# Optimization experiments

Hardware: AMD Instinct MI355X
Metric: run time of the kernel (lower is better)

Reference implementation:

```python
import jax, jax.numpy as jnp
import numpy as np
from jax import lax

B, C, D, H, W = 2, 256, 32, 64, 192
TRAIN_W = 640
DISPS = np.arange(D, dtype=np.float32) * 0.01  # norm_disp_range


def conv1x1(x, w, b):
    # x [B,Cin,H,W], w [Cout,Cin]
    return jnp.einsum('bchw,oc->bohw', x, w) + b[None, :, None, None]


def conv3x3(x, w, b):
    y = lax.conv_general_dilated(x, w, (1, 1), 'SAME',
                                 dimension_numbers=('NCHW', 'OIHW', 'NCHW'))
    return y + b[None, :, None, None]


def warp_volume(x, shift_px):
    """Horizontal bilinear warp with border clamp for each disparity.
    x [B,Cc,H,W], shift_px [B,D] (pixel shift) -> [B,Cc,D,H,W]."""
    Wd = x.shape[3]
    j = jnp.arange(Wd, dtype=x.dtype)
    src = jnp.clip(j[None, None, :] + shift_px[:, :, None], 0.0, Wd - 1.0)  # [B,D,W]
    x0 = jnp.floor(src).astype(jnp.int32)
    x1 = jnp.minimum(x0 + 1, Wd - 1)
    frac = src - x0.astype(src.dtype)  # [B,D,W]

    def one(xb, i0, i1, fb):
        g0 = xb[:, :, i0]  # [Cc,H,D,W]
        g1 = xb[:, :, i1]
        out = g0 * (1.0 - fb) + g1 * fb
        return out.transpose(0, 2, 1, 3)  # [Cc,D,H,W]

    return jax.vmap(one)(x, x0, x1, frac)


def setup_inputs() -> dict:
    key = jax.random.key(0)
    ks = jax.random.split(key, 16)
    f32 = jnp.float32
    inp = {
        't_feat': jax.random.normal(ks[0], (B, C, H, W), f32),
        's_feat': jax.random.normal(ks[1], (B, C, H, W), f32),
        'directs': jnp.ones((B, 1, 1, 1), f32),
        'qw': jax.random.normal(ks[2], (C // 4, C), f32) * 0.05,
        'qb': jax.random.normal(ks[3], (C // 4,), f32) * 0.05,
        'kw': jax.random.normal(ks[4], (C // 4, C), f32) * 0.05,
        'kb': jax.random.normal(ks[5], (C // 4,), f32) * 0.05,
        'vw': jax.random.normal(ks[6], (C // 4, C), f32) * 0.05,
        'vb': jax.random.normal(ks[7], (C // 4,), f32) * 0.05,
        'p1w': jax.random.normal(ks[8], (C // 4, C // 2, 3, 3), f32) * 0.05,
        'p1b': jax.random.normal(ks[9], (C // 4,), f32) * 0.05,
        'p2w': jax.random.normal(ks[10], (D, C // 4, 3, 3), f32) * 0.05,
        'p2b': jax.random.normal(ks[11], (D,), f32) * 0.05,
        'rw': jax.random.normal(ks[12], (C, C + D), f32) * 0.05,
        'rb': jax.random.normal(ks[13], (C,), f32) * 0.05,
        'img_w': TRAIN_W,
    }
    return inp


def reference(t_feat, s_feat, directs, qw, qb, kw, kb, vw, vb,
              p1w, p1b, p2w, p2b, rw, rb, img_w):
    rel_scale = (TRAIN_W / img_w) if img_w != TRAIN_W else 1.0
    q = conv1x1(t_feat, qw, qb)  # [B,C/4,H,W]
    k = conv1x1(s_feat, kw, kb)
    v = conv1x1(s_feat, vw, vb)

    Wd = t_feat.shape[3]
    disps = jnp.asarray(DISPS, t_feat.dtype)
    # normalized shift d*2*rel_scale*directs -> pixels: * (W-1)/2
    shift = disps[None, :] * rel_scale * directs.reshape(-1, 1) * (Wd - 1)  # [B,D]

    wk = warp_volume(k, shift)  # [B,C/4,D,H,W]
    wv = warp_volume(v, shift)

    cq = q.shape[1]
    cost = jnp.einsum('bchw,bcdhw->bdhw', q, wk) / (cq ** 0.5)  # [B,D,H,W]
    norm_cost = jax.nn.softmax(cost, axis=1)
    agg_v = jnp.einsum('bdhw,bcdhw->bchw', norm_cost, wv)  # [B,C/4,H,W]

    h1 = jax.nn.elu(conv3x3(jnp.concatenate([q, agg_v], axis=1), p1w, p1b))
    res_cost = conv3x3(h1, p2w, p2b)  # [B,D,H,W]
    cost = (cost + res_cost) * 0.5
    norm_cost = jax.nn.softmax(cost, axis=1)
    x = jax.nn.elu(conv1x1(jnp.concatenate([t_feat, norm_cost], axis=1), rw, rb))
    return x, cost
```

## Files before the change

### kernel.cpp

```cpp
#include <hip/hip_runtime.h>

#define BB 2
#define CC 256
#define CQ 64
#define DD 32
#define HH 64
#define WW 192
#define HW (HH*WW)
#define NPIX (BB*HW)

typedef __attribute__((ext_vector_type(8))) short bf16x8;
typedef __attribute__((ext_vector_type(4))) float f32x4;

__device__ __forceinline__ float b2f(ushort s){ return __uint_as_float(((uint)s)<<16); }
__device__ __forceinline__ ushort f2b(float f){
    uint u = __float_as_uint(f);
    return (ushort)((u + 0x7fffu + ((u>>16)&1u)) >> 16);
}
__device__ __forceinline__ float eluf(float v){ return v > 0.f ? v : (__expf(v)-1.f); }

__global__ __launch_bounds__(256) void k_prep_feat(
    const float* __restrict__ t_feat, const float* __restrict__ s_feat,
    ushort* __restrict__ Tt, ushort* __restrict__ Ts)
{
    __shared__ ushort sT[64*264];
    int blk = blockIdx.x;
    int which = blk / 384;
    int rem   = blk % 384;
    int b     = rem / 192;
    int tile  = rem % 192;
    int p0    = tile*64;
    const float* src = which ? s_feat : t_feat;
    ushort* dst      = which ? Ts : Tt;
    int tid = threadIdx.x;

    for (int i = tid; i < 2048; i += 256){
        int px  = i & 63;
        int c16 = i >> 6;
        const float* p = src + ((size_t)(b*CC + c16*8))*HW + p0 + px;
        uint u[4];
        #pragma unroll
        for (int j2=0;j2<4;++j2)
            u[j2] = (uint)f2b(p[(size_t)(2*j2)*HW]) | ((uint)f2b(p[(size_t)(2*j2+1)*HW])<<16);
        uint4 q4; q4.x=u[0]; q4.y=u[1]; q4.z=u[2]; q4.w=u[3];
        *(uint4*)&sT[(px*33 + c16)*8] = q4;
    }
    __syncthreads();
    for (int i = tid; i < 2048; i += 256){
        int c16 = i & 31;
        int px  = i >> 5;
        uint4 v = *(const uint4*)&sT[(px*33 + c16)*8];
        *(uint4*)(dst + ((size_t)(b*HW + p0 + px))*CC + c16*8) = v;
    }
}

__global__ __launch_bounds__(256) void k_prep_w(
    const float* __restrict__ qw, const float* __restrict__ qb,
    const float* __restrict__ kw, const float* __restrict__ kb,
    const float* __restrict__ vw, const float* __restrict__ vb,
    const float* __restrict__ p1w, const float* __restrict__ p2w,
    const float* __restrict__ rw,
    ushort* __restrict__ Wqkv, float* __restrict__ bqkv,
    ushort* __restrict__ A1, ushort* __restrict__ A2, ushort* __restrict__ Ar)
{
    int id = blockIdx.x*256 + threadIdx.x;
    if (id < 49152) {
        int o = id / 256, c = id % 256;
        float v = (o<64)? qw[o*256+c] : (o<128)? kw[(o-64)*256+c] : vw[(o-128)*256+c];
        Wqkv[id] = f2b(v);
    } else if (id < 49344) {
        int o = id - 49152;
        bqkv[o] = (o<64)? qb[o] : (o<128)? kb[o-64] : vb[o-128];
    } else if (id < 49344+73728) {
        int i = id - 49344;
        int o = i/1152, r = i%1152, t = r/128, ci = r%128;
        A1[i] = f2b(p1w[(size_t)(o*128+ci)*9 + t]);
    } else if (id < 49344+73728+18432) {
        int i = id - (49344+73728);
        int o = i/576, r = i%576, t = r/64, ci = r%64;
        A2[i] = f2b(p2w[(size_t)(o*64+ci)*9 + t]);
    } else if (id < 49344+73728+18432+73728) {
        int i = id - (49344+73728+18432);
        Ar[i] = f2b(rw[i]);
    }
}

__global__ __launch_bounds__(256) void g_qkv(
    const ushort* __restrict__ Tt, const ushort* __restrict__ Ts,
    const ushort* __restrict__ Wqkv, const float* __restrict__ bqkv,
    ushort* __restrict__ X1, ushort* __restrict__ Vb)
{
    __shared__ ushort sT[32*264];
    __shared__ ushort sS[32*264];
    int tid = threadIdx.x;
    int bid = blockIdx.x;
    int tile = (bid & 7)*96 + (bid >> 3);
    int p0 = tile * 32;

    for (int i = tid; i < 1024; i += 256){
        int px = i >> 5, c16 = i & 31;
        size_t gsrc = ((size_t)(p0 + px))*CC + c16*8;
        *(uint4*)&sT[(px*33 + c16)*8] = *(const uint4*)(Tt + gsrc);
        *(uint4*)&sS[(px*33 + c16)*8] = *(const uint4*)(Ts + gsrc);
    }
    __syncthreads();

    int wv = tid >> 6, lane = tid & 63;
    int lm = lane & 15, lk = lane >> 4;
    f32x4 acc[3][2];
    #pragma unroll
    for (int g=0;g<3;++g){ acc[g][0]=(f32x4){0.f,0.f,0.f,0.f}; acc[g][1]=(f32x4){0.f,0.f,0.f,0.f}; }
    const ushort* Ap = Wqkv + (size_t)(wv*16 + lm)*CC + lk*8;

    #pragma unroll
    for (int k0=0; k0<CC; k0+=32){
        bf16x8 a0 = *(const bf16x8*)(Ap + k0);
        bf16x8 a1 = *(const bf16x8*)(Ap + 64*CC + k0);
        bf16x8 a2 = *(const bf16x8*)(Ap + 128*CC + k0);
        #pragma unroll
        for (int nt=0; nt<2; ++nt){
            int ch = (nt*16+lm)*33 + (k0>>3) + lk;
            bf16x8 bT = *(const bf16x8*)&sT[ch*8];
            bf16x8 bS = *(const bf16x8*)&sS[ch*8];
            acc[0][nt] = __builtin_amdgcn_mfma_f32_16x16x32_bf16(a0, bT, acc[0][nt], 0,0,0);
            acc[1][nt] = __builtin_amdgcn_mfma_f32_16x16x32_bf16(a1, bS, acc[1][nt], 0,0,0);
            acc[2][nt] = __builtin_amdgcn_mfma_f32_16x16x32_bf16(a2, bS, acc[2][nt], 0,0,0);
        }
    }
    int ol = wv*16 + lk*4;
    #pragma unroll
    for (int g=0;g<3;++g){
        int ob = g*64 + ol;
        #pragma unroll
        for (int nt=0; nt<2; ++nt){
            int p = p0 + nt*16 + lm;
            uint u0 = (uint)f2b(acc[g][nt][0]+bqkv[ob])   | ((uint)f2b(acc[g][nt][1]+bqkv[ob+1])<<16);
            uint u1 = (uint)f2b(acc[g][nt][2]+bqkv[ob+2]) | ((uint)f2b(acc[g][nt][3]+bqkv[ob+3])<<16);
            ushort* dst;
            if (g==0)      dst = X1 + (size_t)p*128 + ol;
            else if (g==1) dst = X1 + (size_t)p*128 + 64 + ol;
            else           dst = Vb + (size_t)p*64 + ol;
            *(uint2*)dst = make_uint2(u0, u1);
        }
    }
}

#define BAND 160
#define SROW 161
#define PROW 168
__global__ __launch_bounds__(512) void k_ca(
    const ushort* __restrict__ X1, const ushort* __restrict__ Vb,
    const float* __restrict__ directs, const int* __restrict__ img_w_p,
    float* __restrict__ C1, ushort* __restrict__ Agg)
{
    __shared__ ushort sQ[32*64];
    __shared__ ushort sK[BAND*64];
    __shared__ ushort sV[BAND*64];
    __shared__ float  sS[32*SROW];
    __shared__ ushort sPC[32*PROW];
    int tid = threadIdx.x;
    int j   = blockIdx.x;
    int r8  = j & 7;
    int kk  = j >> 3;
    int sub = kk % 6;
    int rhi = kk / 6;
    int row = rhi*8 + r8;
    int b   = row >> 6;
    int h   = row & 63;
    int w0  = sub * 32;
    size_t rowbase = (size_t)b*HW + (size_t)h*WW;

    for (int i = tid; i < BAND*8; i += 512){
        int x = i >> 3, c8 = i & 7;
        int gx = w0 - 64 + x;
        uint4 kv = make_uint4(0,0,0,0), vv = make_uint4(0,0,0,0);
        if (gx >= 0 && gx < WW){
            kv = *(const uint4*)(X1 + (rowbase+gx)*128 + 64 + c8*8);
            vv = *(const uint4*)(Vb + (rowbase+gx)*64 + c8*8);
        }
        int sw = (x*8 + (c8 ^ (x&7)))*8;
        *(uint4*)&sK[sw] = kv;
        *(uint4*)&sV[sw] = vv;
    }
    if (tid < 256){
        int px = tid >> 3, c8 = tid & 7;
        uint4 qv = *(const uint4*)(X1 + (rowbase + w0 + px)*128 + c8*8);
        *(uint4*)&sQ[(px*8 + (c8 ^ (px&7)))*8] = qv;
    }
    __syncthreads();

    int w8 = tid >> 6, lane = tid & 63;
    int lm = lane & 15, lk = lane >> 4;

    {
        int mt = w8 & 1;
        int qrow = mt*16 + lm;
        for (int nt = (w8 >> 1); nt < 10; nt += 4){
            int xrow = nt*16 + lm;
            f32x4 acc = {0.f,0.f,0.f,0.f};
            #pragma unroll
            for (int kt=0; kt<2; ++kt){
                bf16x8 a = *(const bf16x8*)&sQ[(qrow*8 + ((kt*4+lk) ^ (qrow&7)))*8];
                bf16x8 bbf = *(const bf16x8*)&sK[(xrow*8 + ((kt*4+lk) ^ (xrow&7)))*8];
                acc = __builtin_amdgcn_mfma_f32_16x16x32_bf16(a, bbf, acc, 0,0,0);
            }
            #pragma unroll
            for (int jj=0; jj<4; ++jj)
                sS[(mt*16 + lk*4 + jj)*SROW + xrow] = acc[jj];
        }
    }
    __syncthreads();

    int px  = tid >> 4;
    int l16 = tid & 15;
    int w   = w0 + px;
    size_t n = rowbase + w;
    int imw = img_w_p[0];
    float rel = (imw != 640) ? (640.0f/(float)imw) : 1.0f;
    float sf = 0.01f * rel * directs[b] * 191.0f;
    float wf = (float)w;

    float cost[2]; int xi0[2], xi1[2]; float frk[2];
    #pragma unroll
    for (int t=0; t<2; ++t){
        int d = l16*2 + t;
        float srcx = fminf(fmaxf(wf + (float)d*sf, 0.f), 191.0f);
        int x0 = (int)floorf(srcx);
        int x1 = min(x0+1, WW-1);
        float fr = srcx - (float)x0;
        int i0 = min(max(x0 - w0 + 64, 0), BAND-1);
        int i1 = min(max(x1 - w0 + 64, 0), BAND-1);
        xi0[t] = i0; xi1[t] = i1; frk[t] = fr;
        float s0 = sS[px*SROW + i0];
        float s1 = sS[px*SROW + i1];
        cost[t] = (s0 + fr*(s1-s0)) * 0.125f;
    }
    *(float2*)(C1 + n*DD + l16*2) = make_float2(cost[0], cost[1]);
    float mm = fmaxf(cost[0], cost[1]);
    mm = fmaxf(mm, __shfl_xor(mm, 1));
    mm = fmaxf(mm, __shfl_xor(mm, 2));
    mm = fmaxf(mm, __shfl_xor(mm, 4));
    mm = fmaxf(mm, __shfl_xor(mm, 8));
    float e0 = __expf(cost[0]-mm), e1 = __expf(cost[1]-mm);
    float ss = e0 + e1;
    ss += __shfl_xor(ss, 1);
    ss += __shfl_xor(ss, 2);
    ss += __shfl_xor(ss, 4);
    ss += __shfl_xor(ss, 8);
    float inv = 1.f/ss;
    float p0 = e0*inv, p1 = e1*inv;
    __syncthreads();

    for (int i = tid; i < 32*SROW; i += 512) sS[i] = 0.f;
    __syncthreads();

    {
        float w1a = p0*frk[0], w0a = p0 - w1a;
        float w1b = p1*frk[1], w0b = p1 - w1b;
        atomicAdd(&sS[px*SROW + xi0[0]], w0a);
        atomicAdd(&sS[px*SROW + xi1[0]], w1a);
        atomicAdd(&sS[px*SROW + xi0[1]], w0b);
        atomicAdd(&sS[px*SROW + xi1[1]], w1b);
    }
    __syncthreads();

    #pragma unroll
    for (int q=0; q<10; ++q){
        int xi = l16 + q*16;
        sPC[px*PROW + xi] = f2b(sS[px*SROW + xi]);
    }
    __syncthreads();

    {
        int mi = w8 & 3;
        int ni = w8 >> 2;
        int c  = mi*16 + lm;
        int wr = ni*16 + lm;
        f32x4 acc = {0.f,0.f,0.f,0.f};
        for (int kt=0; kt<5; ++kt){
            bf16x8 a;
            #pragma unroll
            for (int jj=0; jj<8; ++jj){
                int x = kt*32 + lk*8 + jj;
                a[jj] = (short)sV[(x*8 + ((c>>3) ^ (x&7)))*8 + (c&7)];
            }
            bf16x8 bbf = *(const bf16x8*)&sPC[wr*PROW + kt*32 + lk*8];
            acc = __builtin_amdgcn_mfma_f32_16x16x32_bf16(a, bbf, acc, 0,0,0);
        }
        uint u0 = (uint)f2b(acc[0]) | ((uint)f2b(acc[1])<<16);
        uint u1 = (uint)f2b(acc[2]) | ((uint)f2b(acc[3])<<16);
        *(uint2*)(Agg + (rowbase + w0 + wr)*64 + mi*16 + lk*4) = make_uint2(u0, u1);
    }
}

__global__ __launch_bounds__(256) void g_conv1(
    const ushort* __restrict__ X1, const ushort* __restrict__ Agg,
    const ushort* __restrict__ A1, const float* __restrict__ p1b,
    ushort* __restrict__ X2)
{
    __shared__ ushort sB[3*16*34*8];
    int tid = threadIdx.x;
    int wv = tid >> 6, lane = tid & 63;
    int lm = lane & 15, lk = lane >> 4;
    int bid = blockIdx.x;
    int tile = (bid & 7)*96 + (bid >> 3);
    int n0 = tile * 32;
    int b  = n0 / HW;
    int pl = n0 % HW;
    int h  = pl / WW, w0 = pl % WW;

    for (int i = tid; i < 1632; i += 256){
        int dh = i / 544, rem2 = i % 544;
        int c16 = rem2 / 34, x = rem2 % 34;
        int hh = h + dh - 1, wx = w0 + x - 1;
        uint4 val = make_uint4(0,0,0,0);
        if (hh >= 0 && hh < HH && wx >= 0 && wx < WW){
            size_t pix = (size_t)b*HW + (size_t)hh*WW + wx;
            val = (c16 < 8) ? *(const uint4*)(X1 + pix*128 + c16*8)
                            : *(const uint4*)(Agg + pix*64 + (c16-8)*8);
        }
        *(uint4*)&sB[((dh*16 + c16)*34 + x)*8] = val;
    }
    __syncthreads();

    int mw = wv & 1, nw = wv >> 1;
    const ushort* Ap = A1 + (size_t)(mw*32 + lm)*1152 + lk*8;
    f32x4 acc0 = {0.f,0.f,0.f,0.f}, acc1 = {0.f,0.f,0.f,0.f};
    int xb = nw*16 + lm;
    #pragma unroll
    for (int t=0; t<9; ++t){
        int dh = t/3, dw = t%3;
        #pragma unroll
        for (int c0=0; c0<128; c0+=32){
            bf16x8 bb = *(const bf16x8*)&sB[((dh*16 + (c0>>3)+lk)*34 + xb + dw)*8];
            bf16x8 a0 = *(const bf16x8*)(Ap + t*128 + c0);
            bf16x8 a1 = *(const bf16x8*)(Ap + (size_t)16*1152 + t*128 + c0);
            acc0 = __builtin_amdgcn_mfma_f32_16x16x32_bf16(a0, bb, acc0, 0,0,0);
            acc1 = __builtin_amdgcn_mfma_f32_16x16x32_bf16(a1, bb, acc1, 0,0,0);
        }
    }
    int pg = n0 + nw*16 + lm;
    int o0 = mw*32 + lk*4;
    {
        uint u0 = (uint)f2b(eluf(acc0[0]+p1b[o0]))   | ((uint)f2b(eluf(acc0[1]+p1b[o0+1]))<<16);
        uint u1 = (uint)f2b(eluf(acc0[2]+p1b[o0+2])) | ((uint)f2b(eluf(acc0[3]+p1b[o0+3]))<<16);
        *(uint2*)(X2 + (size_t)pg*64 + o0) = make_uint2(u0, u1);
        int o1 = o0 + 16;
        uint u2 = (uint)f2b(eluf(acc1[0]+p1b[o1]))   | ((uint)f2b(eluf(acc1[1]+p1b[o1+1]))<<16);
        uint u3 = (uint)f2b(eluf(acc1[2]+p1b[o1+2])) | ((uint)f2b(eluf(acc1[3]+p1b[o1+3]))<<16);
        *(uint2*)(X2 + (size_t)pg*64 + o1) = make_uint2(u2, u3);
    }
}

__global__ __launch_bounds__(256) void g_conv2(
    const ushort* __restrict__ X2, const ushort* __restrict__ A2,
    const float* __restrict__ p2b, const float* __restrict__ C1,
    float* __restrict__ cost_out)
{
    __shared__ ushort sB[3*8*34*8];
    int tid = threadIdx.x;
    int wv = tid >> 6, lane = tid & 63;
    int lm = lane & 15, lk = lane >> 4;
    int bid = blockIdx.x;
    int tile = (bid & 7)*96 + (bid >> 3);
    int n0 = tile * 32;
    int b  = n0 / HW;
    int pl = n0 % HW;
    int h  = pl / WW, w0 = pl % WW;

    for (int i = tid; i < 816; i += 256){
        int dh = i / 272, rem2 = i % 272;
        int c16 = rem2 / 34, x = rem2 % 34;
        int hh = h + dh - 1, wx = w0 + x - 1;
        uint4 val = make_uint4(0,0,0,0);
        if (hh >= 0 && hh < HH && wx >= 0 && wx < WW)
            val = *(const uint4*)(X2 + ((size_t)b*HW + (size_t)hh*WW + wx)*64 + c16*8);
        *(uint4*)&sB[((dh*8 + c16)*34 + x)*8] = val;
    }
    __syncthreads();

    int mw = wv & 1, nw = wv >> 1;
    const ushort* Ap = A2 + (size_t)(mw*16 + lm)*576 + lk*8;
    f32x4 acc = {0.f,0.f,0.f,0.f};
    int xb = nw*16 + lm;
    #pragma unroll
    for (int t=0; t<9; ++t){
        int dh = t/3, dw = t%3;
        #pragma unroll
        for (int c0=0; c0<64; c0+=32){
            bf16x8 bb = *(const bf16x8*)&sB[((dh*8 + (c0>>3)+lk)*34 + xb + dw)*8];
            bf16x8 a  = *(const bf16x8*)(Ap + t*64 + c0);
            acc = __builtin_amdgcn_mfma_f32_16x16x32_bf16(a, bb, acc, 0,0,0);
        }
    }
    int pg = n0 + nw*16 + lm;
    int pll = pg % HW;
    int o = mw*16 + lk*4;
    f32x4 cv = *(const f32x4*)(C1 + (size_t)pg*DD + o);
    #pragma unroll
    for (int j=0;j<4;++j)
        cost_out[((size_t)(b*DD + o + j))*HW + pll] = (cv[j] + acc[j] + p2b[o+j]) * 0.5f;
}

__global__ __launch_bounds__(256) void k_sm2(
    const float* __restrict__ cost_out, ushort* __restrict__ NC)
{
    int n = blockIdx.x*256 + threadIdx.x;
    int b = n / HW, pl = n % HW;
    const float* cp = cost_out + (size_t)b*DD*HW + pl;
    float v[DD]; float m = -1e30f;
    #pragma unroll
    for (int d=0; d<DD; ++d){ v[d] = cp[(size_t)d*HW]; m = fmaxf(m, v[d]); }
    float s = 0.f;
    #pragma unroll
    for (int d=0; d<DD; ++d){ v[d] = __expf(v[d]-m); s += v[d]; }
    float inv = 1.f/s;
    ushort* op = NC + (size_t)n*DD;
    #pragma unroll
    for (int d8=0; d8<4; ++d8){
        uint u[4];
        #pragma unroll
        for (int j2=0;j2<4;++j2)
            u[j2] = (uint)f2b(v[d8*8+j2*2]*inv) | ((uint)f2b(v[d8*8+j2*2+1]*inv)<<16);
        uint4 q4; q4.x=u[0]; q4.y=u[1]; q4.z=u[2]; q4.w=u[3];
        *(uint4*)(op + d8*8) = q4;
    }
}

__global__ __launch_bounds__(256) void g_final(
    const ushort* __restrict__ Tt, const ushort* __restrict__ NC,
    const ushort* __restrict__ Ar, const float* __restrict__ rb,
    float* __restrict__ xout)
{
    __shared__ ushort sT[32*264];
    __shared__ ushort sN[32*40];
    int tid = threadIdx.x;
    int bid = blockIdx.x;
    int tile = (bid & 7)*96 + (bid >> 3);
    int p0 = tile * 32;

    for (int i = tid; i < 1024; i += 256){
        int px = i >> 5, c16 = i & 31;
        *(uint4*)&sT[(px*33 + c16)*8] = *(const uint4*)(Tt + ((size_t)(p0+px))*CC + c16*8);
    }
    if (tid < 128){
        int px = tid >> 2, c4 = tid & 3;
        *(uint4*)&sN[(px*5 + c4)*8] = *(const uint4*)(NC + ((size_t)(p0+px))*DD + c4*8);
    }
    __syncthreads();

    int wv = tid >> 6, lane = tid & 63;
    int lm = lane & 15, lk = lane >> 4;
    f32x4 acc[4][2];
    #pragma unroll
    for (int mi=0;mi<4;++mi){ acc[mi][0]=(f32x4){0.f,0.f,0.f,0.f}; acc[mi][1]=(f32x4){0.f,0.f,0.f,0.f}; }
    const ushort* Ap = Ar + (size_t)(wv*64 + lm)*288 + lk*8;

    #pragma unroll
    for (int k0=0; k0<288; k0+=32){
        bf16x8 a[4];
        #pragma unroll
        for (int mi=0;mi<4;++mi) a[mi] = *(const bf16x8*)(Ap + (size_t)mi*16*288 + k0);
        #pragma unroll
        for (int nt=0; nt<2; ++nt){
            int prow = nt*16 + lm;
            bf16x8 bb = (k0 < 256) ? *(const bf16x8*)&sT[(prow*33 + (k0>>3) + lk)*8]
                                   : *(const bf16x8*)&sN[(prow*5 + lk)*8];
            #pragma unroll
            for (int mi=0;mi<4;++mi)
                acc[mi][nt] = __builtin_amdgcn_mfma_f32_16x16x32_bf16(a[mi], bb, acc[mi][nt], 0,0,0);
        }
    }
    #pragma unroll
    for (int mi=0;mi<4;++mi){
        int o = wv*64 + mi*16 + lk*4;
        #pragma unroll
        for (int nt=0; nt<2; ++nt){
            int p = p0 + nt*16 + lm;
            int b = p / HW, pl = p % HW;
            #pragma unroll
            for (int j=0;j<4;++j)
                xout[((size_t)(b*CC + o + j))*HW + pl] = eluf(acc[mi][nt][j] + rb[o+j]);
        }
    }
}

extern "C" void kernel_launch(void* const* d_in, const int* in_sizes, int n_in,
                              void* d_out, int out_size, void* d_ws, size_t ws_size,
                              hipStream_t stream)
{
    const float* t_feat = (const float*)d_in[0];
    const float* s_feat = (const float*)d_in[1];
    const float* directs= (const float*)d_in[2];
    const float* qw = (const float*)d_in[3];
    const float* qb = (const float*)d_in[4];
    const float* kw = (const float*)d_in[5];
    const float* kb = (const float*)d_in[6];
    const float* vw = (const float*)d_in[7];
    const float* vb = (const float*)d_in[8];
    const float* p1w= (const float*)d_in[9];
    const float* p1b= (const float*)d_in[10];
    const float* p2w= (const float*)d_in[11];
    const float* p2b= (const float*)d_in[12];
    const float* rw = (const float*)d_in[13];
    const float* rb = (const float*)d_in[14];
    const int* img_w= (const int*)d_in[15];

    char* wsb = (char*)d_ws;
    ushort* Tt   = (ushort*)(wsb + 0);
    char*  tsreg = wsb + 12582912;
    ushort* Ts   = (ushort*)tsreg;
    ushort* X2   = (ushort*)tsreg;
    float*  C1   = (float*)(tsreg + 3145728);
    ushort* Agg  = (ushort*)(tsreg + 6291456);
    ushort* X1   = (ushort*)(wsb + 25165824);
    ushort* Vb   = (ushort*)(wsb + 31457280);
    ushort* NC   = (ushort*)(wsb + 31457280);
    ushort* Wqkv = (ushort*)(wsb + 34603008);
    float*  bqkv = (float*) (wsb + 34701312);
    ushort* A1   = (ushort*)(wsb + 34702336);
    ushort* A2   = (ushort*)(wsb + 34849792);
    ushort* Ar   = (ushort*)(wsb + 34886656);
    if (ws_size < 35034112) return;

    float* xout     = (float*)d_out;
    float* cost_out = xout + (size_t)BB*CC*HW;

    k_prep_feat<<<768, 256, 0, stream>>>(t_feat, s_feat, Tt, Ts);
    k_prep_w  <<<841,  256, 0, stream>>>(qw,qb,kw,kb,vw,vb,p1w,p2w,rw, Wqkv,bqkv,A1,A2,Ar);
    g_qkv     <<<768,  256, 0, stream>>>(Tt, Ts, Wqkv, bqkv, X1, Vb);
    k_ca      <<<768,  512, 0, stream>>>(X1, Vb, directs, img_w, C1, Agg);
    g_conv1   <<<768,  256, 0, stream>>>(X1, Agg, A1, p1b, X2);
    g_conv2   <<<768,  256, 0, stream>>>(X2, A2, p2b, C1, cost_out);
    k_sm2     <<<96,   256, 0, stream>>>(cost_out, NC);
    g_final   <<<768,  256, 0, stream>>>(Tt, NC, Ar, rb, xout);
}
```

Baseline: 112.9 us.

## Store V channel-major, transpose score tile, fuse second softmax into conv2

The QKV kernel now writes V in channel-major layout, so the attention kernel loads V rows contiguously and feeds MFMA A-operands with vector LDS loads instead of per-element gathers. The score tile in shared memory is transposed so each MFMA result is stored as one vector write. The separate softmax kernel is removed and its work folded into g_conv2 through a shared-memory staging tile, which avoids re-reading cost_out and one launch. The risks are the strided scattered writes of VbT in g_qkv and the removed index clamps in the attention kernel.

```diff
diff --git a/kernel.cpp b/kernel.cpp
--- a/kernel.cpp
+++ b/kernel.cpp
@@ -88,7 +88,7 @@
 __global__ __launch_bounds__(256) void g_qkv(
     const ushort* __restrict__ Tt, const ushort* __restrict__ Ts,
     const ushort* __restrict__ Wqkv, const float* __restrict__ bqkv,
-    ushort* __restrict__ X1, ushort* __restrict__ Vb)
+    ushort* __restrict__ X1, ushort* __restrict__ VbT)
 {
     __shared__ ushort sT[32*264];
     __shared__ ushort sS[32*264];
@@ -129,35 +129,40 @@
     }
     int ol = wv*16 + lk*4;
     #pragma unroll
-    for (int g=0;g<3;++g){
-        int ob = g*64 + ol;
-        #pragma unroll
-        for (int nt=0; nt<2; ++nt){
-            int p = p0 + nt*16 + lm;
-            uint u0 = (uint)f2b(acc[g][nt][0]+bqkv[ob])   | ((uint)f2b(acc[g][nt][1]+bqkv[ob+1])<<16);
-            uint u1 = (uint)f2b(acc[g][nt][2]+bqkv[ob+2]) | ((uint)f2b(acc[g][nt][3]+bqkv[ob+3])<<16);
-            ushort* dst;
-            if (g==0)      dst = X1 + (size_t)p*128 + ol;
-            else if (g==1) dst = X1 + (size_t)p*128 + 64 + ol;
-            else           dst = Vb + (size_t)p*64 + ol;
-            *(uint2*)dst = make_uint2(u0, u1);
-        }
+    for (int nt=0; nt<2; ++nt){
+        int p = p0 + nt*16 + lm;
+        {
+            int ob = ol;
+            uint u0 = (uint)f2b(acc[0][nt][0]+bqkv[ob])   | ((uint)f2b(acc[0][nt][1]+bqkv[ob+1])<<16);
+            uint u1 = (uint)f2b(acc[0][nt][2]+bqkv[ob+2]) | ((uint)f2b(acc[0][nt][3]+bqkv[ob+3])<<16);
+            *(uint2*)(X1 + (size_t)p*128 + ol) = make_uint2(u0, u1);
+        }
+        {
+            int ob = 64 + ol;
+            uint u0 = (uint)f2b(acc[1][nt][0]+bqkv[ob])   | ((uint)f2b(acc[1][nt][1]+bqkv[ob+1])<<16);
+            uint u1 = (uint)f2b(acc[1][nt][2]+bqkv[ob+2]) | ((uint)f2b(acc[1][nt][3]+bqkv[ob+3])<<16);
+            *(uint2*)(X1 + (size_t)p*128 + 64 + ol) = make_uint2(u0, u1);
+        }
+        #pragma unroll
+        for (int j=0;j<4;++j)
+            VbT[(size_t)(ol+j)*NPIX + p] = f2b(acc[2][nt][j] + bqkv[128 + ol + j]);
     }
 }
 
 #define BAND 160
-#define SROW 161
-#define PROW 168
+#define VTS 168
+#define STS 36
+#define PFS 164
 __global__ __launch_bounds__(512) void k_ca(
-    const ushort* __restrict__ X1, const ushort* __restrict__ Vb,
+    const ushort* __restrict__ X1, const ushort* __restrict__ VbT,
     const float* __restrict__ directs, const int* __restrict__ img_w_p,
     float* __restrict__ C1, ushort* __restrict__ Agg)
 {
     __shared__ ushort sQ[32*64];
     __shared__ ushort sK[BAND*64];
-    __shared__ ushort sV[BAND*64];
-    __shared__ float  sS[32*SROW];
-    __shared__ ushort sPC[32*PROW];
+    __shared__ ushort sVT[64*VTS];
+    __shared__ float  sF[BAND*STS];
+    __shared__ ushort sPC[32*VTS];
     int tid = threadIdx.x;
     int j   = blockIdx.x;
     int r8  = j & 7;
@@ -173,14 +178,18 @@
     for (int i = tid; i < BAND*8; i += 512){
         int x = i >> 3, c8 = i & 7;
         int gx = w0 - 64 + x;
-        uint4 kv = make_uint4(0,0,0,0), vv = make_uint4(0,0,0,0);
-        if (gx >= 0 && gx < WW){
+        uint4 kv = make_uint4(0,0,0,0);
+        if (gx >= 0 && gx < WW)
             kv = *(const uint4*)(X1 + (rowbase+gx)*128 + 64 + c8*8);
-            vv = *(const uint4*)(Vb + (rowbase+gx)*64 + c8*8);
-        }
-        int sw = (x*8 + (c8 ^ (x&7)))*8;
-        *(uint4*)&sK[sw] = kv;
-        *(uint4*)&sV[sw] = vv;
+        *(uint4*)&sK[(x*8 + (c8 ^ (x&7)))*8] = kv;
+    }
+    for (int i = tid; i < 64*20; i += 512){
+        int c = i / 20, k2 = i % 20;
+        int gx = w0 - 64 + k2*8;
+        uint4 vv = make_uint4(0,0,0,0);
+        if (gx >= 0 && gx < WW)
+            vv = *(const uint4*)(VbT + (size_t)c*NPIX + rowbase + gx);
+        *(uint4*)&sVT[c*VTS + k2*8] = vv;
     }
     if (tid < 256){
         int px = tid >> 3, c8 = tid & 7;
@@ -204,9 +213,7 @@
                 bf16x8 bbf = *(const bf16x8*)&sK[(xrow*8 + ((kt*4+lk) ^ (xrow&7)))*8];
                 acc = __builtin_amdgcn_mfma_f32_16x16x32_bf16(a, bbf, acc, 0,0,0);
             }
-            #pragma unroll
-            for (int jj=0; jj<4; ++jj)
-                sS[(mt*16 + lk*4 + jj)*SROW + xrow] = acc[jj];
+            *(f32x4*)&sF[xrow*STS + mt*16 + lk*4] = acc;
         }
     }
     __syncthreads();
@@ -228,11 +235,11 @@
         int x0 = (int)floorf(srcx);
         int x1 = min(x0+1, WW-1);
         float fr = srcx - (float)x0;
-        int i0 = min(max(x0 - w0 + 64, 0), BAND-1);
-        int i1 = min(max(x1 - w0 + 64, 0), BAND-1);
+        int i0 = x0 - w0 + 64;
+        int i1 = x1 - w0 + 64;
         xi0[t] = i0; xi1[t] = i1; frk[t] = fr;
-        float s0 = sS[px*SROW + i0];
-        float s1 = sS[px*SROW + i1];
+        float s0 = sF[i0*STS + px];
+        float s1 = sF[i1*STS + px];
         cost[t] = (s0 + fr*(s1-s0)) * 0.125f;
     }
     *(float2*)(C1 + n*DD + l16*2) = make_float2(cost[0], cost[1]);
@@ -251,23 +258,27 @@
     float p0 = e0*inv, p1 = e1*inv;
     __syncthreads();
 
-    for (int i = tid; i < 32*SROW; i += 512) sS[i] = 0.f;
+    for (int i = tid; i < (32*PFS)/4; i += 512)
+        *(f32x4*)&sF[i*4] = (f32x4){0.f,0.f,0.f,0.f};
     __syncthreads();
 
     {
         float w1a = p0*frk[0], w0a = p0 - w1a;
         float w1b = p1*frk[1], w0b = p1 - w1b;
-        atomicAdd(&sS[px*SROW + xi0[0]], w0a);
-        atomicAdd(&sS[px*SROW + xi1[0]], w1a);
-        atomicAdd(&sS[px*SROW + xi0[1]], w0b);
-        atomicAdd(&sS[px*SROW + xi1[1]], w1b);
-    }
-    __syncthreads();
-
-    #pragma unroll
-    for (int q=0; q<10; ++q){
-        int xi = l16 + q*16;
-        sPC[px*PROW + xi] = f2b(sS[px*SROW + xi]);
+        atomicAdd(&sF[px*PFS + xi0[0]], w0a);
+        atomicAdd(&sF[px*PFS + xi1[0]], w1a);
+        atomicAdd(&sF[px*PFS + xi0[1]], w0b);
+        atomicAdd(&sF[px*PFS + xi1[1]], w1b);
+    }
+    __syncthreads();
+
+    {
+        int base = l16*10;
+        #pragma unroll
+        for (int q=0; q<5; ++q){
+            float2 v2 = *(const float2*)&sF[px*PFS + base + q*2];
+            *(uint*)&sPC[px*VTS + base + q*2] = (uint)f2b(v2.x) | ((uint)f2b(v2.y)<<16);
+        }
     }
     __syncthreads();
 
@@ -277,14 +288,10 @@
         int c  = mi*16 + lm;
         int wr = ni*16 + lm;
         f32x4 acc = {0.f,0.f,0.f,0.f};
+        #pragma unroll
         for (int kt=0; kt<5; ++kt){
-            bf16x8 a;
-            #pragma unroll
-            for (int jj=0; jj<8; ++jj){
-                int x = kt*32 + lk*8 + jj;
-                a[jj] = (short)sV[(x*8 + ((c>>3) ^ (x&7)))*8 + (c&7)];
-            }
-            bf16x8 bbf = *(const bf16x8*)&sPC[wr*PROW + kt*32 + lk*8];
+            bf16x8 a   = *(const bf16x8*)&sVT[c*VTS + kt*32 + lk*8];
+            bf16x8 bbf = *(const bf16x8*)&sPC[wr*VTS + kt*32 + lk*8];
             acc = __builtin_amdgcn_mfma_f32_16x16x32_bf16(a, bbf, acc, 0,0,0);
         }
         uint u0 = (uint)f2b(acc[0]) | ((uint)f2b(acc[1])<<16);
@@ -355,9 +362,10 @@
 __global__ __launch_bounds__(256) void g_conv2(
     const ushort* __restrict__ X2, const ushort* __restrict__ A2,
     const float* __restrict__ p2b, const float* __restrict__ C1,
-    float* __restrict__ cost_out)
+    float* __restrict__ cost_out, ushort* __restrict__ NC)
 {
     __shared__ ushort sB[3*8*34*8];
+    __shared__ float  sO[32*36];
     int tid = threadIdx.x;
     int wv = tid >> 6, lane = tid & 63;
     int lm = lane & 15, lk = lane >> 4;
@@ -397,33 +405,33 @@
     int pll = pg % HW;
     int o = mw*16 + lk*4;
     f32x4 cv = *(const f32x4*)(C1 + (size_t)pg*DD + o);
-    #pragma unroll
-    for (int j=0;j<4;++j)
-        cost_out[((size_t)(b*DD + o + j))*HW + pll] = (cv[j] + acc[j] + p2b[o+j]) * 0.5f;
-}
-
-__global__ __launch_bounds__(256) void k_sm2(
-    const float* __restrict__ cost_out, ushort* __restrict__ NC)
-{
-    int n = blockIdx.x*256 + threadIdx.x;
-    int b = n / HW, pl = n % HW;
-    const float* cp = cost_out + (size_t)b*DD*HW + pl;
-    float v[DD]; float m = -1e30f;
-    #pragma unroll
-    for (int d=0; d<DD; ++d){ v[d] = cp[(size_t)d*HW]; m = fmaxf(m, v[d]); }
-    float s = 0.f;
-    #pragma unroll
-    for (int d=0; d<DD; ++d){ v[d] = __expf(v[d]-m); s += v[d]; }
-    float inv = 1.f/s;
-    ushort* op = NC + (size_t)n*DD;
-    #pragma unroll
-    for (int d8=0; d8<4; ++d8){
-        uint u[4];
-        #pragma unroll
-        for (int j2=0;j2<4;++j2)
-            u[j2] = (uint)f2b(v[d8*8+j2*2]*inv) | ((uint)f2b(v[d8*8+j2*2+1]*inv)<<16);
-        uint4 q4; q4.x=u[0]; q4.y=u[1]; q4.z=u[2]; q4.w=u[3];
-        *(uint4*)(op + d8*8) = q4;
+    f32x4 outv;
+    #pragma unroll
+    for (int j=0;j<4;++j){
+        outv[j] = (cv[j] + acc[j] + p2b[o+j]) * 0.5f;
+        cost_out[((size_t)(b*DD + o + j))*HW + pll] = outv[j];
+    }
+    *(f32x4*)&sO[(nw*16 + lm)*36 + o] = outv;
+    __syncthreads();
+
+    {
+        int px = tid >> 3;
+        int g  = tid & 7;
+        f32x4 v = *(const f32x4*)&sO[px*36 + g*4];
+        float m = fmaxf(fmaxf(v[0],v[1]), fmaxf(v[2],v[3]));
+        m = fmaxf(m, __shfl_xor(m, 1));
+        m = fmaxf(m, __shfl_xor(m, 2));
+        m = fmaxf(m, __shfl_xor(m, 4));
+        float e[4]; float s = 0.f;
+        #pragma unroll
+        for (int j=0;j<4;++j){ e[j] = __expf(v[j]-m); s += e[j]; }
+        s += __shfl_xor(s, 1);
+        s += __shfl_xor(s, 2);
+        s += __shfl_xor(s, 4);
+        float invs = 1.f/s;
+        uint u0 = (uint)f2b(e[0]*invs) | ((uint)f2b(e[1]*invs)<<16);
+        uint u1 = (uint)f2b(e[2]*invs) | ((uint)f2b(e[3]*invs)<<16);
+        *(uint2*)(NC + (size_t)(n0 + px)*DD + g*4) = make_uint2(u0, u1);
     }
 }
 
@@ -514,7 +522,7 @@
     float*  C1   = (float*)(tsreg + 3145728);
     ushort* Agg  = (ushort*)(tsreg + 6291456);
     ushort* X1   = (ushort*)(wsb + 25165824);
-    ushort* Vb   = (ushort*)(wsb + 31457280);
+    ushort* VbT  = (ushort*)(wsb + 31457280);
     ushort* NC   = (ushort*)(wsb + 31457280);
     ushort* Wqkv = (ushort*)(wsb + 34603008);
     float*  bqkv = (float*) (wsb + 34701312);
@@ -528,10 +536,9 @@
 
     k_prep_feat<<<768, 256, 0, stream>>>(t_feat, s_feat, Tt, Ts);
     k_prep_w  <<<841,  256, 0, stream>>>(qw,qb,kw,kb,vw,vb,p1w,p2w,rw, Wqkv,bqkv,A1,A2,Ar);
-    g_qkv     <<<768,  256, 0, stream>>>(Tt, Ts, Wqkv, bqkv, X1, Vb);
-    k_ca      <<<768,  512, 0, stream>>>(X1, Vb, directs, img_w, C1, Agg);
+    g_qkv     <<<768,  256, 0, stream>>>(Tt, Ts, Wqkv, bqkv, X1, VbT);
+    k_ca      <<<768,  512, 0, stream>>>(X1, VbT, directs, img_w, C1, Agg);
     g_conv1   <<<768,  256, 0, stream>>>(X1, Agg, A1, p1b, X2);
-    g_conv2   <<<768,  256, 0, stream>>>(X2, A2, p2b, C1, cost_out);
-    k_sm2     <<<96,   256, 0, stream>>>(cost_out, NC);
+    g_conv2   <<<768,  256, 0, stream>>>(X2, A2, p2b, C1, cost_out, NC);
     g_final   <<<768,  256, 0, stream>>>(Tt, NC, Ar, rb, xout);
 }
```

After: 110.2 us. 2.4% less time.
